# Kernel optimization log

Hardware: AMD Instinct MI355X
Metric: run time of the kernel (lower is better)

## Reference

```python
import jax, jax.numpy as jnp
import numpy as np
import math

EMBED_DIM = 1024
NUM_HEADS = 8
HEAD_DIM = EMBED_DIM // NUM_HEADS
N, L, S = 4, 1024, 1024


def setup_inputs() -> dict:
    key = jax.random.key(0)
    ks = jax.random.split(key, 12)
    E = EMBED_DIM
    # xavier_uniform for square (E,E): bound = sqrt(6/(E+E))
    bound = math.sqrt(6.0 / (E + E))
    def xavier(k):
        return jax.random.uniform(k, (E, E), jnp.float32, -bound, bound)
    return {
        "query": jax.random.normal(ks[0], (N, L, E), jnp.float32),
        "key": jax.random.normal(ks[1], (N, S, E), jnp.float32),
        "value": jax.random.normal(ks[2], (N, S, E), jnp.float32),
        "key_padding_mask": jnp.zeros((N, S), dtype=bool),
        "attn_mask": jnp.zeros((L, S), dtype=bool),
        "q_w": xavier(ks[3]), "q_b": jnp.zeros((E,), jnp.float32),
        "k_w": xavier(ks[4]), "k_b": jnp.zeros((E,), jnp.float32),
        "v_w": xavier(ks[5]), "v_b": jnp.zeros((E,), jnp.float32),
        "out_w": xavier(ks[6]), "out_b": jnp.zeros((E,), jnp.float32),
    }


def _mha(query, key, value, key_padding_mask, attn_mask,
         q_w, q_b, k_w, k_b, v_w, v_b, out_w, out_b):
    H, D, E = NUM_HEADS, HEAD_DIM, EMBED_DIM
    # batch_first=True -> transpose to (L, N, E)
    query = jnp.swapaxes(query, 0, 1)  # (L, N, E)
    key = jnp.swapaxes(key, 0, 1)      # (S, N, E)
    value = jnp.swapaxes(value, 0, 1)  # (S, N, E)
    Lq, Nb, _ = query.shape
    Sk = key.shape[0]

    q = query @ q_w.T + q_b
    k = key @ k_w.T + k_b
    v = value @ v_w.T + v_b

    # (L,N,H,D) -> (N,H,L,D) -> (N*H, L, D); batch index = n*H + h
    q = q.reshape(Lq, Nb, H, D).transpose(1, 2, 0, 3).reshape(Nb * H, Lq, D)
    k = k.reshape(Sk, Nb, H, D).transpose(1, 2, 0, 3).reshape(Nb * H, Sk, D)
    v = v.reshape(Sk, Nb, H, D).transpose(1, 2, 0, 3).reshape(Nb * H, Sk, D)

    scores = jnp.einsum('bld,bsd->bls', q, k) / math.sqrt(D)  # (N*H, L, S)
    neg_inf = jnp.asarray(-jnp.inf, scores.dtype)
    if attn_mask is not None:
        scores = jnp.where(attn_mask[None, :, :], neg_inf, scores)
    if key_padding_mask is not None:
        kpm = jnp.broadcast_to(key_padding_mask[:, None, None, :],
                               (Nb, H, 1, Sk)).reshape(Nb * H, 1, Sk)
        scores = jnp.where(kpm, neg_inf, scores)

    attn = jax.nn.softmax(scores, axis=-1)
    out = jnp.einsum('bls,bsd->bld', attn, v)  # (N*H, L, D)

    # FAITHFUL reproduction of the original (buggy when N != H) output reshape:
    # reshape(H, N, L, D) on an N-major batch dim, then transpose(0,2),
    # transpose(1,2), reshape(L, N, E).
    out = out.reshape(H, Nb, Lq, D)
    out = jnp.swapaxes(out, 0, 2)   # (L, N, H, D)
    out = jnp.swapaxes(out, 1, 2)   # (L, H, N, D)
    out = out.reshape(Lq, Nb, E)
    out = out @ out_w.T + out_b
    return jnp.swapaxes(out, 0, 1)  # (N, L, E)


def reference(query, key, value, key_padding_mask, attn_mask,
              q_w, q_b, k_w, k_b, v_w, v_b, out_w, out_b):
    return _mha(query, key, value, key_padding_mask, attn_mask,
                q_w, q_b, k_w, k_b, v_w, v_b, out_w, out_b)
```

## Files before the change

### kernel.cpp

```cpp
#include <hip/hip_runtime.h>
#include <hip/hip_bf16.h>

typedef __bf16 bf16;
typedef __bf16 bf16x4 __attribute__((ext_vector_type(4)));
typedef __bf16 bf16x8 __attribute__((ext_vector_type(8)));
typedef float  f32x4  __attribute__((ext_vector_type(4)));

#define GLD_LDS(g, l) __builtin_amdgcn_global_load_lds(                        \
    (const __attribute__((address_space(1))) unsigned int*)(g),                \
    (__attribute__((address_space(3))) unsigned int*)(l), 16, 0, 0)

struct CvtSegs {
  const float* src[7];
  bf16* dst[7];
  int n8[7];
  int total8;
};

__global__ __launch_bounds__(256) void cvt_all(CvtSegs s) {
  int i = blockIdx.x * 256 + threadIdx.x;
  if (i >= s.total8) return;
  int seg = 0, off = i;
  while (off >= s.n8[seg]) { off -= s.n8[seg]; ++seg; }
  const float4* sp = reinterpret_cast<const float4*>(s.src[seg]);
  float4 a = sp[2 * off], b = sp[2 * off + 1];
  bf16x8 o;
  o[0] = (bf16)a.x; o[1] = (bf16)a.y; o[2] = (bf16)a.z; o[3] = (bf16)a.w;
  o[4] = (bf16)b.x; o[5] = (bf16)b.y; o[6] = (bf16)b.z; o[7] = (bf16)b.w;
  reinterpret_cast<bf16x8*>(s.dst[seg])[off] = o;
}

template <int MODE>
__global__ __launch_bounds__(256) void gemm_bt(
    const bf16* __restrict__ A0, const bf16* __restrict__ A1, const bf16* __restrict__ A2,
    const bf16* __restrict__ B0, const bf16* __restrict__ B1, const bf16* __restrict__ B2,
    const float* __restrict__ bias0, const float* __restrict__ bias1, const float* __restrict__ bias2,
    void* __restrict__ C0, void* __restrict__ C1, void* __restrict__ C2) {
  const int f = blockIdx.x + (blockIdx.y << 3) + (blockIdx.z << 8);
  const int nwg = (int)(gridDim.x * gridDim.y * gridDim.z);
  const int cpx = nwg >> 3;
  const int g = (f & 7) * cpx + (f >> 3);
  const int bn = g & 7;
  const int bm = (g >> 3) & 31;
  const int z = g >> 8;

  const bf16* A = (z == 0) ? A0 : (z == 1) ? A1 : A2;
  const bf16* B = (z == 0) ? B0 : (z == 1) ? B1 : B2;
  const float* bias = (z == 0) ? bias0 : (z == 1) ? bias1 : bias2;
  void* C = (z == 0) ? C0 : (z == 1) ? C1 : C2;

  const int t = threadIdx.x;
  const int lane = t & 63, w = t >> 6;
  const int lr = lane & 15, lk = lane >> 4;
  const int wm = w >> 1, wn = w & 1;

  __shared__ __align__(16) bf16 As[128 * 32];
  __shared__ __align__(16) bf16 Bs[128 * 32];

  f32x4 acc[4][4];
#pragma unroll
  for (int m = 0; m < 4; ++m)
#pragma unroll
    for (int n = 0; n < 4; ++n) acc[m][n] = {0.f, 0.f, 0.f, 0.f};

  for (int kt = 0; kt < 32; ++kt) {
#pragma unroll
    for (int p = 0; p < 2; ++p) {
      const int idx = p * 256 + t;
      const int row = idx >> 2;
      const int col = (idx & 3) * 8;
      const int ldso = (p * 256 + (t & ~63)) * 8;
      GLD_LDS(A + (size_t)(bm * 128 + row) * 1024 + kt * 32 + col, &As[ldso]);
      GLD_LDS(B + (size_t)(bn * 128 + row) * 1024 + kt * 32 + col, &Bs[ldso]);
    }
    __syncthreads();

    bf16x8 af[4], bfr[4];
#pragma unroll
    for (int m = 0; m < 4; ++m)
      af[m] = *(const bf16x8*)&As[(wm * 64 + m * 16 + lr) * 32 + lk * 8];
#pragma unroll
    for (int n = 0; n < 4; ++n)
      bfr[n] = *(const bf16x8*)&Bs[(wn * 64 + n * 16 + lr) * 32 + lk * 8];
#pragma unroll
    for (int m = 0; m < 4; ++m)
#pragma unroll
      for (int n = 0; n < 4; ++n)
        acc[m][n] = __builtin_amdgcn_mfma_f32_16x16x32_bf16(af[m], bfr[n], acc[m][n], 0, 0, 0);
    __syncthreads();
  }

#pragma unroll
  for (int m = 0; m < 4; ++m)
#pragma unroll
    for (int n = 0; n < 4; ++n) {
      const int gc = bn * 128 + wn * 64 + n * 16 + lr;
      const float bv = bias[gc];
      if (MODE == 0 && z == 2) {
        bf16x4 pk;
#pragma unroll
        for (int r = 0; r < 4; ++r) {
          pk[r] = (bf16)(acc[m][n][r] + bv);
        }
        const int gr0 = bm * 128 + wm * 64 + m * 16 + lk * 4;
        const int nb = gr0 >> 10, l0 = gr0 & 1023;
        const int hh = gc >> 7, d = gc & 127;
        *(bf16x4*)((bf16*)C + ((size_t)(nb * 8 + hh) * 128 + d) * 1024 + l0) = pk;
      } else {
#pragma unroll
        for (int r = 0; r < 4; ++r) {
          const int gr = bm * 128 + wm * 64 + m * 16 + lk * 4 + r;
          const float val = acc[m][n][r] + bv;
          if constexpr (MODE == 0) {
            ((bf16*)C)[(size_t)gr * 1024 + gc] = (bf16)val;
          } else {
            ((float*)C)[(size_t)(gr & 3) * 1048576 + (size_t)(gr >> 2) * 1024 + gc] = val;
          }
        }
      }
    }
}

__global__ __launch_bounds__(256, 4) void attn_fwd(const bf16* __restrict__ Qg,
                                                   const bf16* __restrict__ Kg,
                                                   const bf16* __restrict__ Vtg,
                                                   bf16* __restrict__ X) {
  const int bh = blockIdx.x;
  const int qt = blockIdx.y;
  const int n = bh >> 3, h = bh & 7;
  const int t = threadIdx.x;
  const int lane = t & 63, w = t >> 6;
  const int lr = lane & 15, lk = lane >> 4;
  const int qsub = w & 1, kvh = w >> 1;

  __shared__ __align__(16) char smem[40960];
  char* KsB = smem;
  char* VsB = smem + 16384;
  char* PbB = smem + 32768 + w * 2048;

  const float scale2 = 0.12754136351576995f;

  const bf16* qp = Qg + ((size_t)n * 1024 + qt * 32 + qsub * 16 + lr) * 1024 + h * 128;
  bf16x8 qf[4];
#pragma unroll
  for (int kc = 0; kc < 4; ++kc) {
    bf16x8 raw = *(const bf16x8*)(qp + kc * 32 + lk * 8);
#pragma unroll
    for (int j = 0; j < 8; ++j) qf[kc][j] = (bf16)((float)raw[j] * scale2);
  }

  float mrow[4], srow[4];
  f32x4 oacc[8];
#pragma unroll
  for (int r = 0; r < 4; ++r) { mrow[r] = -1e30f; srow[r] = 0.f; }
#pragma unroll
  for (int nd = 0; nd < 8; ++nd) oacc[nd] = {0.f, 0.f, 0.f, 0.f};

  for (int i = 0; i < 16; ++i) {
    __syncthreads();

#pragma unroll
    for (int g = 0; g < 4; ++g) {
      const int r = w * 16 + g * 4 + lk;
      const int c = (lane & 15) ^ (r & 7);
      GLD_LDS(Kg + ((size_t)n * 1024 + i * 64 + r) * 1024 + h * 128 + c * 8,
              KsB + (w * 16 + g * 4) * 256);
    }
#pragma unroll
    for (int g = 0; g < 4; ++g) {
      const int d = w * 32 + g * 8 + (lane >> 3);
      const int c = (lane & 7) ^ (d & 7);
      GLD_LDS(Vtg + ((size_t)bh * 128 + d) * 1024 + i * 64 + c * 8,
              VsB + (w * 32 + g * 8) * 128);
    }
    asm volatile("s_waitcnt vmcnt(0)" ::: "memory");
    __syncthreads();

    f32x4 s4[2];
    s4[0] = {0.f, 0.f, 0.f, 0.f};
    s4[1] = {0.f, 0.f, 0.f, 0.f};
    __builtin_amdgcn_s_setprio(1);
#pragma unroll
    for (int kc = 0; kc < 4; ++kc)
#pragma unroll
      for (int nf = 0; nf < 2; ++nf) {
        const int s = kvh * 32 + nf * 16 + lr;
        const int byte = (s * 256 + kc * 64 + lk * 16) ^ ((s & 7) << 4);
        bf16x8 kf = *(const bf16x8*)(KsB + byte);
        s4[nf] = __builtin_amdgcn_mfma_f32_16x16x32_bf16(qf[kc], kf, s4[nf], 0, 0, 0);
      }
    __builtin_amdgcn_s_setprio(0);

    float pv[2][4];
    int okf = 1;
#pragma unroll
    for (int r = 0; r < 4; ++r) {
      pv[0][r] = s4[0][r];
      pv[1][r] = s4[1][r];
      okf &= (fmaxf(pv[0][r], pv[1][r]) <= mrow[r] + 8.0f) ? 1 : 0;
    }
    if (!__all(okf)) {
#pragma unroll
      for (int r = 0; r < 4; ++r) {
        float mx = fmaxf(pv[0][r], pv[1][r]);
        mx = fmaxf(mx, __shfl_xor(mx, 1, 16));
        mx = fmaxf(mx, __shfl_xor(mx, 2, 16));
        mx = fmaxf(mx, __shfl_xor(mx, 4, 16));
        mx = fmaxf(mx, __shfl_xor(mx, 8, 16));
        const float mnew = fmaxf(mrow[r], mx);
        const float fold = __builtin_amdgcn_exp2f(mrow[r] - mnew);
        mrow[r] = mnew;
        srow[r] *= fold;
#pragma unroll
        for (int nd = 0; nd < 8; ++nd) oacc[nd][r] *= fold;
      }
    }
#pragma unroll
    for (int r = 0; r < 4; ++r) {
      const float e0 = __builtin_amdgcn_exp2f(pv[0][r] - mrow[r]);
      const float e1 = __builtin_amdgcn_exp2f(pv[1][r] - mrow[r]);
      pv[0][r] = e0; pv[1][r] = e1;
      srow[r] += e0 + e1;
    }

#pragma unroll
    for (int nf = 0; nf < 2; ++nf)
#pragma unroll
      for (int r = 0; r < 4; ++r) {
        const int q = lk * 4 + r, s = nf * 16 + lr;
        const int byte = (q * 128 + s * 2) ^ ((q & 7) << 4);
        *(bf16*)(PbB + byte) = (bf16)pv[nf][r];
      }
    asm volatile("s_waitcnt lgkmcnt(0)" ::: "memory");
    __builtin_amdgcn_sched_barrier(0);

    const int pbyte = (lr * 128 + lk * 16) ^ ((lr & 7) << 4);
    bf16x8 pf = *(const bf16x8*)(PbB + pbyte);
    __builtin_amdgcn_s_setprio(1);
#pragma unroll
    for (int nd = 0; nd < 8; ++nd) {
      const int d = nd * 16 + lr;
      const int vbyte = (d * 128 + kvh * 64 + lk * 16) ^ ((d & 7) << 4);
      bf16x8 vf = *(const bf16x8*)(VsB + vbyte);
      oacc[nd] = __builtin_amdgcn_mfma_f32_16x16x32_bf16(pf, vf, oacc[nd], 0, 0, 0);
    }
    __builtin_amdgcn_s_setprio(0);
  }

#pragma unroll
  for (int r = 0; r < 4; ++r) {
    float s = srow[r];
    s += __shfl_xor(s, 1, 16);
    s += __shfl_xor(s, 2, 16);
    s += __shfl_xor(s, 4, 16);
    s += __shfl_xor(s, 8, 16);
    srow[r] = s;
  }

  __syncthreads();
  float* Ol = (float*)smem + qsub * (16 * 128);
  float* Ms = (float*)(smem + 16384) + qsub * 32;
  if (kvh == 1) {
#pragma unroll
    for (int nd = 0; nd < 8; ++nd)
#pragma unroll
      for (int r = 0; r < 4; ++r)
        Ol[(lk * 4 + r) * 128 + nd * 16 + lr] = oacc[nd][r];
    if (lr == 0) {
#pragma unroll
      for (int r = 0; r < 4; ++r) {
        Ms[(lk * 4 + r) * 2 + 0] = mrow[r];
        Ms[(lk * 4 + r) * 2 + 1] = srow[r];
      }
    }
  }
  __syncthreads();
  if (kvh == 0) {
    float rs1[4], rs2[4];
#pragma unroll
    for (int r = 0; r < 4; ++r) {
      const float m2 = Ms[(lk * 4 + r) * 2 + 0];
      const float s2 = Ms[(lk * 4 + r) * 2 + 1];
      const float mN = fmaxf(mrow[r], m2);
      const float w1 = __builtin_amdgcn_exp2f(mrow[r] - mN);
      const float w2 = __builtin_amdgcn_exp2f(m2 - mN);
      const float rd = 1.f / (srow[r] * w1 + s2 * w2);
      rs1[r] = w1 * rd; rs2[r] = w2 * rd;
    }
#pragma unroll
    for (int nd = 0; nd < 8; ++nd)
#pragma unroll
      for (int r = 0; r < 4; ++r) {
        const float o = oacc[nd][r] * rs1[r] +
                        Ol[(lk * 4 + r) * 128 + nd * 16 + lr] * rs2[r];
        const int l = qt * 32 + qsub * 16 + lk * 4 + r;
        const int d = nd * 16 + lr;
        X[((size_t)l * 32 + bh) * 128 + d] = (bf16)o;
      }
  }
}

extern "C" void kernel_launch(void* const* d_in, const int* in_sizes, int n_in,
                              void* d_out, int out_size, void* d_ws, size_t ws_size,
                              hipStream_t stream) {
  const float* query = (const float*)d_in[0];
  const float* key_i = (const float*)d_in[1];
  const float* value = (const float*)d_in[2];
  const float* q_w = (const float*)d_in[5];
  const float* q_b = (const float*)d_in[6];
  const float* k_w = (const float*)d_in[7];
  const float* k_b = (const float*)d_in[8];
  const float* v_w = (const float*)d_in[9];
  const float* v_b = (const float*)d_in[10];
  const float* o_w = (const float*)d_in[11];
  const float* o_b = (const float*)d_in[12];

  char* p = (char*)d_ws;
  bf16* qin = (bf16*)p; p += (size_t)4096 * 1024 * 2;
  bf16* kin = (bf16*)p; p += (size_t)4096 * 1024 * 2;
  bf16* vin = (bf16*)p; p += (size_t)4096 * 1024 * 2;
  bf16* wq  = (bf16*)p; p += (size_t)1024 * 1024 * 2;
  bf16* wk  = (bf16*)p; p += (size_t)1024 * 1024 * 2;
  bf16* wv  = (bf16*)p; p += (size_t)1024 * 1024 * 2;
  bf16* wo  = (bf16*)p; p += (size_t)1024 * 1024 * 2;
  bf16* Qb  = (bf16*)p; p += (size_t)4096 * 1024 * 2;
  bf16* Kb  = (bf16*)p; p += (size_t)4096 * 1024 * 2;
  bf16* Vtg = (bf16*)p; p += (size_t)4096 * 1024 * 2;
  bf16* Xb  = (bf16*)p; p += (size_t)4096 * 1024 * 2;

  CvtSegs cs;
  cs.src[0] = query; cs.dst[0] = qin; cs.n8[0] = 524288;
  cs.src[1] = key_i; cs.dst[1] = kin; cs.n8[1] = 524288;
  cs.src[2] = value; cs.dst[2] = vin; cs.n8[2] = 524288;
  cs.src[3] = q_w;   cs.dst[3] = wq;  cs.n8[3] = 131072;
  cs.src[4] = k_w;   cs.dst[4] = wk;  cs.n8[4] = 131072;
  cs.src[5] = v_w;   cs.dst[5] = wv;  cs.n8[5] = 131072;
  cs.src[6] = o_w;   cs.dst[6] = wo;  cs.n8[6] = 131072;
  cs.total8 = 3 * 524288 + 4 * 131072;
  cvt_all<<<(cs.total8 + 255) / 256, 256, 0, stream>>>(cs);

  gemm_bt<0><<<dim3(8, 32, 3), 256, 0, stream>>>(qin, kin, vin, wq, wk, wv,
                                                 q_b, k_b, v_b, Qb, Kb, Vtg);
  attn_fwd<<<dim3(32, 32), 256, 0, stream>>>(Qb, Kb, Vtg, Xb);
  gemm_bt<1><<<dim3(8, 32, 1), 256, 0, stream>>>(Xb, Xb, Xb, wo, wo, wo,
                                                 o_b, o_b, o_b, d_out, d_out, d_out);
}
```

Measured before the change: 115.7 us.

## Fuse fp32-to-bf16 conversion into GEMM loads with register-staged double buffering

Removes the separate conversion kernel and its bf16 workspace copies. The GEMMs now read fp32 activations and weights directly, convert them to bf16 in registers, and write them to padded, double-buffered LDS. The next k-tile is prefetched into registers while the current tile's MFMAs run. The trade-off is that fp32 operands are re-read and re-converted by every tile that uses them, which doubles global read bytes per tile, and the register pressure is higher.

```diff
diff --git a/kernel.cpp b/kernel.cpp
--- a/kernel.cpp
+++ b/kernel.cpp
@@ -10,30 +10,17 @@
     (const __attribute__((address_space(1))) unsigned int*)(g),                \
     (__attribute__((address_space(3))) unsigned int*)(l), 16, 0, 0)
 
-struct CvtSegs {
-  const float* src[7];
-  bf16* dst[7];
-  int n8[7];
-  int total8;
-};
-
-__global__ __launch_bounds__(256) void cvt_all(CvtSegs s) {
-  int i = blockIdx.x * 256 + threadIdx.x;
-  if (i >= s.total8) return;
-  int seg = 0, off = i;
-  while (off >= s.n8[seg]) { off -= s.n8[seg]; ++seg; }
-  const float4* sp = reinterpret_cast<const float4*>(s.src[seg]);
-  float4 a = sp[2 * off], b = sp[2 * off + 1];
+static __device__ __forceinline__ bf16x8 cvt8(float4 a, float4 b) {
   bf16x8 o;
   o[0] = (bf16)a.x; o[1] = (bf16)a.y; o[2] = (bf16)a.z; o[3] = (bf16)a.w;
   o[4] = (bf16)b.x; o[5] = (bf16)b.y; o[6] = (bf16)b.z; o[7] = (bf16)b.w;
-  reinterpret_cast<bf16x8*>(s.dst[seg])[off] = o;
+  return o;
 }
 
 template <int MODE>
-__global__ __launch_bounds__(256) void gemm_bt(
-    const bf16* __restrict__ A0, const bf16* __restrict__ A1, const bf16* __restrict__ A2,
-    const bf16* __restrict__ B0, const bf16* __restrict__ B1, const bf16* __restrict__ B2,
+__global__ __launch_bounds__(256, 3) void gemm_f(
+    const void* __restrict__ A0, const void* __restrict__ A1, const void* __restrict__ A2,
+    const float* __restrict__ B0, const float* __restrict__ B1, const float* __restrict__ B2,
     const float* __restrict__ bias0, const float* __restrict__ bias1, const float* __restrict__ bias2,
     void* __restrict__ C0, void* __restrict__ C1, void* __restrict__ C2) {
   const int f = blockIdx.x + (blockIdx.y << 3) + (blockIdx.z << 8);
@@ -44,8 +31,8 @@
   const int bm = (g >> 3) & 31;
   const int z = g >> 8;
 
-  const bf16* A = (z == 0) ? A0 : (z == 1) ? A1 : A2;
-  const bf16* B = (z == 0) ? B0 : (z == 1) ? B1 : B2;
+  const void* A = (z == 0) ? A0 : (z == 1) ? A1 : A2;
+  const float* B = (z == 0) ? B0 : (z == 1) ? B1 : B2;
   const float* bias = (z == 0) ? bias0 : (z == 1) ? bias1 : bias2;
   void* C = (z == 0) ? C0 : (z == 1) ? C1 : C2;
 
@@ -54,8 +41,44 @@
   const int lr = lane & 15, lk = lane >> 4;
   const int wm = w >> 1, wn = w & 1;
 
-  __shared__ __align__(16) bf16 As[128 * 32];
-  __shared__ __align__(16) bf16 Bs[128 * 32];
+  __shared__ __align__(16) bf16 As[2][128 * 40];
+  __shared__ __align__(16) bf16 Bs[2][128 * 40];
+
+  const int arow = t >> 1;
+  const int ac16 = (t & 1) * 16;
+
+  float4 ra[4], rb[4];
+  bf16x8 rab[2];
+
+  auto loads = [&](int kt) {
+    if constexpr (MODE == 0) {
+      const float4* Af = (const float4*)((const float*)A +
+          (size_t)(bm * 128 + arow) * 1024 + kt * 32 + ac16);
+#pragma unroll
+      for (int i = 0; i < 4; ++i) ra[i] = Af[i];
+    } else {
+      const bf16x8* Ab = (const bf16x8*)((const bf16*)A +
+          (size_t)(bm * 128 + arow) * 1024 + kt * 32 + ac16);
+#pragma unroll
+      for (int i = 0; i < 2; ++i) rab[i] = Ab[i];
+    }
+    const float4* Bf = (const float4*)(B + (size_t)(bn * 128 + arow) * 1024 + kt * 32 + ac16);
+#pragma unroll
+    for (int i = 0; i < 4; ++i) rb[i] = Bf[i];
+  };
+  auto store = [&](int buf) {
+    bf16* Ad = &As[buf][arow * 40 + ac16];
+    if constexpr (MODE == 0) {
+      *(bf16x8*)Ad = cvt8(ra[0], ra[1]);
+      *(bf16x8*)(Ad + 8) = cvt8(ra[2], ra[3]);
+    } else {
+      *(bf16x8*)Ad = rab[0];
+      *(bf16x8*)(Ad + 8) = rab[1];
+    }
+    bf16* Bd = &Bs[buf][arow * 40 + ac16];
+    *(bf16x8*)Bd = cvt8(rb[0], rb[1]);
+    *(bf16x8*)(Bd + 8) = cvt8(rb[2], rb[3]);
+  };
 
   f32x4 acc[4][4];
 #pragma unroll
@@ -63,31 +86,30 @@
 #pragma unroll
     for (int n = 0; n < 4; ++n) acc[m][n] = {0.f, 0.f, 0.f, 0.f};
 
+  loads(0);
+  store(0);
+  __syncthreads();
+
+  int c = 0;
   for (int kt = 0; kt < 32; ++kt) {
-#pragma unroll
-    for (int p = 0; p < 2; ++p) {
-      const int idx = p * 256 + t;
-      const int row = idx >> 2;
-      const int col = (idx & 3) * 8;
-      const int ldso = (p * 256 + (t & ~63)) * 8;
-      GLD_LDS(A + (size_t)(bm * 128 + row) * 1024 + kt * 32 + col, &As[ldso]);
-      GLD_LDS(B + (size_t)(bn * 128 + row) * 1024 + kt * 32 + col, &Bs[ldso]);
-    }
-    __syncthreads();
+    if (kt != 31) loads(kt + 1);
 
     bf16x8 af[4], bfr[4];
 #pragma unroll
     for (int m = 0; m < 4; ++m)
-      af[m] = *(const bf16x8*)&As[(wm * 64 + m * 16 + lr) * 32 + lk * 8];
+      af[m] = *(const bf16x8*)&As[c][(wm * 64 + m * 16 + lr) * 40 + lk * 8];
 #pragma unroll
     for (int n = 0; n < 4; ++n)
-      bfr[n] = *(const bf16x8*)&Bs[(wn * 64 + n * 16 + lr) * 32 + lk * 8];
+      bfr[n] = *(const bf16x8*)&Bs[c][(wn * 64 + n * 16 + lr) * 40 + lk * 8];
 #pragma unroll
     for (int m = 0; m < 4; ++m)
 #pragma unroll
       for (int n = 0; n < 4; ++n)
         acc[m][n] = __builtin_amdgcn_mfma_f32_16x16x32_bf16(af[m], bfr[n], acc[m][n], 0, 0, 0);
+
+    if (kt != 31) store(c ^ 1);
     __syncthreads();
+    c ^= 1;
   }
 
 #pragma unroll
@@ -316,32 +338,16 @@
   const float* o_b = (const float*)d_in[12];
 
   char* p = (char*)d_ws;
-  bf16* qin = (bf16*)p; p += (size_t)4096 * 1024 * 2;
-  bf16* kin = (bf16*)p; p += (size_t)4096 * 1024 * 2;
-  bf16* vin = (bf16*)p; p += (size_t)4096 * 1024 * 2;
-  bf16* wq  = (bf16*)p; p += (size_t)1024 * 1024 * 2;
-  bf16* wk  = (bf16*)p; p += (size_t)1024 * 1024 * 2;
-  bf16* wv  = (bf16*)p; p += (size_t)1024 * 1024 * 2;
-  bf16* wo  = (bf16*)p; p += (size_t)1024 * 1024 * 2;
   bf16* Qb  = (bf16*)p; p += (size_t)4096 * 1024 * 2;
   bf16* Kb  = (bf16*)p; p += (size_t)4096 * 1024 * 2;
   bf16* Vtg = (bf16*)p; p += (size_t)4096 * 1024 * 2;
   bf16* Xb  = (bf16*)p; p += (size_t)4096 * 1024 * 2;
 
-  CvtSegs cs;
-  cs.src[0] = query; cs.dst[0] = qin; cs.n8[0] = 524288;
-  cs.src[1] = key_i; cs.dst[1] = kin; cs.n8[1] = 524288;
-  cs.src[2] = value; cs.dst[2] = vin; cs.n8[2] = 524288;
-  cs.src[3] = q_w;   cs.dst[3] = wq;  cs.n8[3] = 131072;
-  cs.src[4] = k_w;   cs.dst[4] = wk;  cs.n8[4] = 131072;
-  cs.src[5] = v_w;   cs.dst[5] = wv;  cs.n8[5] = 131072;
-  cs.src[6] = o_w;   cs.dst[6] = wo;  cs.n8[6] = 131072;
-  cs.total8 = 3 * 524288 + 4 * 131072;
-  cvt_all<<<(cs.total8 + 255) / 256, 256, 0, stream>>>(cs);
-
-  gemm_bt<0><<<dim3(8, 32, 3), 256, 0, stream>>>(qin, kin, vin, wq, wk, wv,
-                                                 q_b, k_b, v_b, Qb, Kb, Vtg);
+  gemm_f<0><<<dim3(8, 32, 3), 256, 0, stream>>>(query, key_i, value,
+                                                q_w, k_w, v_w,
+                                                q_b, k_b, v_b, Qb, Kb, Vtg);
   attn_fwd<<<dim3(32, 32), 256, 0, stream>>>(Qb, Kb, Vtg, Xb);
-  gemm_bt<1><<<dim3(8, 32, 1), 256, 0, stream>>>(Xb, Xb, Xb, wo, wo, wo,
-                                                 o_b, o_b, o_b, d_out, d_out, d_out);
+  gemm_f<1><<<dim3(8, 32, 1), 256, 0, stream>>>(Xb, Xb, Xb,
+                                                o_w, o_w, o_w,
+                                                o_b, o_b, o_b, d_out, d_out, d_out);
 }
```

New measurement: 135.6 us. +17.3%, slower.

## Triple-buffer projection GEMM LDS tiles with async prefetch two stages ahead

Applied to the files above, without the earlier changes.

The projection GEMM now keeps three LDS buffers for A and B and issues global-to-LDS loads two k-tiles ahead. It synchronises with explicit vmcnt waits and a single barrier per iteration instead of two __syncthreads. This is meant to hide global load latency behind the MFMA work. It also raises wave priority around the MFMA block. LDS use triples to 48KB per block, which may reduce occupancy.

```diff
diff --git a/kernel.cpp b/kernel.cpp
--- a/kernel.cpp
+++ b/kernel.cpp
@@ -54,40 +54,63 @@
   const int lr = lane & 15, lk = lane >> 4;
   const int wm = w >> 1, wn = w & 1;
 
-  __shared__ __align__(16) bf16 As[128 * 32];
-  __shared__ __align__(16) bf16 Bs[128 * 32];
-
-  f32x4 acc[4][4];
-#pragma unroll
-  for (int m = 0; m < 4; ++m)
-#pragma unroll
-    for (int n = 0; n < 4; ++n) acc[m][n] = {0.f, 0.f, 0.f, 0.f};
-
-  for (int kt = 0; kt < 32; ++kt) {
+  __shared__ __align__(16) bf16 As[3][128 * 32];
+  __shared__ __align__(16) bf16 Bs[3][128 * 32];
+
+  auto STAGE = [&](bf16* Ad, bf16* Bd, int kt) {
 #pragma unroll
     for (int p = 0; p < 2; ++p) {
       const int idx = p * 256 + t;
       const int row = idx >> 2;
       const int col = (idx & 3) * 8;
       const int ldso = (p * 256 + (t & ~63)) * 8;
-      GLD_LDS(A + (size_t)(bm * 128 + row) * 1024 + kt * 32 + col, &As[ldso]);
-      GLD_LDS(B + (size_t)(bn * 128 + row) * 1024 + kt * 32 + col, &Bs[ldso]);
-    }
-    __syncthreads();
+      GLD_LDS(A + (size_t)(bm * 128 + row) * 1024 + kt * 32 + col, Ad + ldso);
+      GLD_LDS(B + (size_t)(bn * 128 + row) * 1024 + kt * 32 + col, Bd + ldso);
+    }
+  };
+
+  f32x4 acc[4][4];
+#pragma unroll
+  for (int m = 0; m < 4; ++m)
+#pragma unroll
+    for (int n = 0; n < 4; ++n) acc[m][n] = {0.f, 0.f, 0.f, 0.f};
+
+  bf16 *a0 = As[0], *a1 = As[1], *a2 = As[2];
+  bf16 *b0 = Bs[0], *b1 = Bs[1], *b2 = Bs[2];
+
+  STAGE(a0, b0, 0);
+  STAGE(a1, b1, 1);
+  asm volatile("s_waitcnt vmcnt(4)" ::: "memory");
+  __builtin_amdgcn_s_barrier();
+
+  for (int kt = 0; kt < 32; ++kt) {
+    if (kt < 30) STAGE(a2, b2, kt + 2);
+    __builtin_amdgcn_sched_barrier(0);
 
     bf16x8 af[4], bfr[4];
 #pragma unroll
     for (int m = 0; m < 4; ++m)
-      af[m] = *(const bf16x8*)&As[(wm * 64 + m * 16 + lr) * 32 + lk * 8];
+      af[m] = *(const bf16x8*)&a0[(wm * 64 + m * 16 + lr) * 32 + lk * 8];
 #pragma unroll
     for (int n = 0; n < 4; ++n)
-      bfr[n] = *(const bf16x8*)&Bs[(wn * 64 + n * 16 + lr) * 32 + lk * 8];
+      bfr[n] = *(const bf16x8*)&b0[(wn * 64 + n * 16 + lr) * 32 + lk * 8];
+    __builtin_amdgcn_s_setprio(1);
 #pragma unroll
     for (int m = 0; m < 4; ++m)
 #pragma unroll
       for (int n = 0; n < 4; ++n)
         acc[m][n] = __builtin_amdgcn_mfma_f32_16x16x32_bf16(af[m], bfr[n], acc[m][n], 0, 0, 0);
-    __syncthreads();
+    __builtin_amdgcn_s_setprio(0);
+
+    if (kt < 30) {
+      asm volatile("s_waitcnt vmcnt(4)" ::: "memory");
+    } else if (kt == 30) {
+      asm volatile("s_waitcnt vmcnt(0)" ::: "memory");
+    }
+    if (kt < 31) __builtin_amdgcn_s_barrier();
+
+    bf16* ta = a0; a0 = a1; a1 = a2; a2 = ta;
+    bf16* tb = b0; b0 = b1; b1 = b2; b2 = tb;
   }
 
 #pragma unroll
```

After: 118.2 us. 2.2% more time.
